# Optimization experiments

Hardware: AMD Instinct MI355X
Metric: run time of the kernel (lower is better)

The kernel has to match this reference:

```python
import jax, jax.numpy as jnp
import numpy as np

GROUP_SIZE = 16777216   # 2**24, output length
PROJ_RATIO = 0.25
INNER = 4194304         # int(GROUP_SIZE * PROJ_RATIO) = 2**22
PADDED = 16777216       # 2**ceil(log2(GROUP_SIZE)) = 2**24
D = 2048                # int(sqrt(INNER))
RANK = 16
ALPHA = 1.0
SCALING = ALPHA / RANK


def setup_inputs() -> dict:
    key = jax.random.key(0)
    kA, kB = jax.random.split(key)
    # LoRA factors (B is zero-init in torch; use small random values so the
    # pipeline produces non-trivial numbers — the math is identical).
    A = jax.random.normal(kA, (RANK, D), dtype=jnp.float32) * 0.02
    Bw = jax.random.normal(kB, (D, RANK), dtype=jnp.float32) * 0.02
    # Fastfood buffers, deterministic as in FastfoodProjection(seed=42)
    rng = np.random.RandomState(42)
    G = jnp.asarray(rng.randn(PADDED), dtype=jnp.float32)
    sign = jnp.asarray(rng.choice([-1, 1], size=PADDED), dtype=jnp.float32)
    perm = jnp.asarray(rng.permutation(PADDED), dtype=jnp.int32)
    return {"A": A, "Bw": Bw, "G": G, "sign": sign, "perm": perm}


def fwht(x):
    """Fast Walsh-Hadamard transform over the last (only) axis, normalized
    by 1/sqrt(n). Same butterfly order as the torch loop: step doubles from 1,
    within each block of 2*step: (a, b) -> (a+b, a-b)."""
    n = x.shape[-1]  # static python int, power of two
    step = 1
    while step < n:
        y = x.reshape(-1, 2, step)               # blocks of 2*step
        x = jnp.concatenate([y[:, :1] + y[:, 1:], y[:, :1] - y[:, 1:]],
                            axis=1).reshape(-1)
        step *= 2
    return x * np.float32(1.0 / np.sqrt(n))


def reference(A, Bw, G, sign, perm):
    # LoRA delta: (D, RANK) @ (RANK, D) * alpha/rank -> (D, D)
    delta = (Bw @ A) * jnp.float32(SCALING)
    flat = delta.reshape(-1)                     # (INNER,)
    flat = jnp.pad(flat, (0, PADDED - INNER))    # zero-pad to 2**24
    # Fastfood: H * G * Pi * H * B
    out = fwht(flat * sign)
    out = out[perm] * G
    out = fwht(out)
    # out_features == GROUP_SIZE == PADDED, so the slice/pad in
    # SuperLoRAGroup.forward is a no-op here; keep it for faithfulness.
    return out[:GROUP_SIZE]
```

## Files before the change

kernel.cpp:

```cpp
#include <hip/hip_runtime.h>


#define THREADS 1024

typedef float vf4 __attribute__((ext_vector_type(4)));
typedef int vi4 __attribute__((ext_vector_type(4)));

constexpr float kScaling = 0.0625f;
constexpr float kNorm = 5.9604644775390625e-8f;

__device__ __forceinline__ void fwht16(float r[16]) {
#pragma unroll
  for (int s = 1; s < 16; s <<= 1) {
#pragma unroll
    for (int i = 0; i < 16; i++) {
      if (!(i & s)) {
        float a = r[i];
        float b = r[i | s];
        r[i] = a + b;
        r[i | s] = a - b;
      }
    }
  }
}

template <bool NT>
__device__ __forceinline__ void fwht_lo_rounds(float* lds, int t, vf4* dst4) {
  vf4* lds4 = (vf4*)lds;
  {
    float r[16];
#pragma unroll
    for (int q = 0; q < 4; q++) {
      vf4 v = lds4[t * 4 + q];
#pragma unroll
      for (int c = 0; c < 4; c++) r[4 * q + c] = v[c];
    }
    fwht16(r);
#pragma unroll
    for (int q = 0; q < 4; q++) {
      vf4 v;
#pragma unroll
      for (int c = 0; c < 4; c++) v[c] = r[4 * q + c];
      lds4[t * 4 + q] = v;
    }
  }
  __syncthreads();
  {
    const int c = (t & 15) | ((t >> 4) << 8);
    float r[16];
#pragma unroll
    for (int k = 0; k < 16; k++) r[k] = lds[c + (k << 4)];
    fwht16(r);
#pragma unroll
    for (int k = 0; k < 16; k++) lds[c + (k << 4)] = r[k];
  }
  __syncthreads();
  {
    const int c = (t & 255) | ((t >> 8) << 12);
    float r[16];
#pragma unroll
    for (int k = 0; k < 16; k++) r[k] = lds[c + (k << 8)];
    fwht16(r);
#pragma unroll
    for (int k = 0; k < 16; k++) lds[c + (k << 8)] = r[k];
  }
  __syncthreads();
  {
    vf4 v0 = lds4[t + 0 * 1024];
    vf4 v1 = lds4[t + 1 * 1024];
    vf4 v2 = lds4[t + 2 * 1024];
    vf4 v3 = lds4[t + 3 * 1024];
    vf4 e0 = v0 + v1, e1 = v0 - v1;
    vf4 e2 = v2 + v3, e3 = v2 - v3;
    vf4 o0 = e0 + e2, o1 = e1 + e3, o2 = e0 - e2, o3 = e1 - e3;
    if (NT) {
      __builtin_nontemporal_store(o0, &dst4[t + 0 * 1024]);
      __builtin_nontemporal_store(o1, &dst4[t + 1 * 1024]);
      __builtin_nontemporal_store(o2, &dst4[t + 2 * 1024]);
      __builtin_nontemporal_store(o3, &dst4[t + 3 * 1024]);
    } else {
      dst4[t + 0 * 1024] = o0;
      dst4[t + 1 * 1024] = o1;
      dst4[t + 2 * 1024] = o2;
      dst4[t + 3 * 1024] = o3;
    }
  }
}

__global__ __launch_bounds__(THREADS) void k1_build_fwht_lo(
    const float* __restrict__ A, const float* __restrict__ Bw,
    const float* __restrict__ sgn, float* __restrict__ W) {
  __shared__ float lds[16384];
  const int t = threadIdx.x;
  const int blk = blockIdx.x;
  const unsigned base = (unsigned)blk << 14;

  float a0[16], a1[16];
#pragma unroll
  for (int k = 0; k < 16; k++) {
    a0[k] = A[k * 2048 + t];
    a1[k] = A[k * 2048 + t + 1024];
  }
  const int r0 = blk * 8;
#pragma unroll
  for (int rl = 0; rl < 8; rl++) {
    float s0 = 0.f, s1 = 0.f;
#pragma unroll
    for (int k = 0; k < 16; k++) {
      float b = Bw[(r0 + rl) * 16 + k];
      s0 += b * a0[k];
      s1 += b * a1[k];
    }
    const int l0 = rl * 2048 + t;
    const int l1 = l0 + 1024;
    lds[l0] = s0 * kScaling * sgn[base + l0];
    lds[l1] = s1 * kScaling * sgn[base + l1];
  }
  __syncthreads();
  fwht_lo_rounds<false>(lds, t, (vf4*)W + ((unsigned)blk << 12));
}

__global__ __launch_bounds__(THREADS) void k_fwht_mid(float* __restrict__ buf) {
  __shared__ float lds[16384];
  vf4* lds4 = (vf4*)lds;
  const int t = threadIdx.x;
  const int seg = blockIdx.x >> 8;
  const int c0 = (blockIdx.x & 255) * 16;
  vf4* B4 = (vf4*)buf + ((unsigned)seg << 20);
#pragma unroll
  for (int m = 0; m < 4; m++) {
    const int idx4 = t + THREADS * m;
    const int row = idx4 >> 4, c4 = idx4 & 15;
    lds4[idx4] = B4[row * 4096 + c0 + c4];
  }
  __syncthreads();
  const int c4 = t & 15;
  const int f = t >> 4;
#pragma unroll
  for (int r = 0; r < 4; r++) {
    const int m = 1 << (2 * r);
    int rows[4];
#pragma unroll
    for (int k2 = 0; k2 < 4; k2++)
      rows[k2] = (f & (m - 1)) + k2 * m + (f >> (2 * r)) * (m << 2);
    vf4 v0 = lds4[rows[0] * 16 + c4];
    vf4 v1 = lds4[rows[1] * 16 + c4];
    vf4 v2 = lds4[rows[2] * 16 + c4];
    vf4 v3 = lds4[rows[3] * 16 + c4];
    vf4 e0 = v0 + v1, e1 = v0 - v1;
    vf4 e2 = v2 + v3, e3 = v2 - v3;
    vf4 o0 = e0 + e2, o1 = e1 + e3, o2 = e0 - e2, o3 = e1 - e3;
    if (r < 3) {
      lds4[rows[0] * 16 + c4] = o0;
      lds4[rows[1] * 16 + c4] = o1;
      lds4[rows[2] * 16 + c4] = o2;
      lds4[rows[3] * 16 + c4] = o3;
      __syncthreads();
    } else {
      B4[rows[0] * 4096 + c0 + c4] = o0;
      B4[rows[1] * 4096 + c0 + c4] = o1;
      B4[rows[2] * 4096 + c0 + c4] = o2;
      B4[rows[3] * 4096 + c0 + c4] = o3;
    }
  }
}

__global__ __launch_bounds__(THREADS) void k3_perm_fwht_lo(
    const float* __restrict__ W, const int* __restrict__ perm,
    const float* __restrict__ G, float* __restrict__ out) {
  __shared__ float lds[16384];
  const int t = threadIdx.x;
  const unsigned base4 = (unsigned)blockIdx.x << 12;
  const vi4* P4 = (const vi4*)perm + base4;
  const vf4* G4 = (const vf4*)G + base4;
  int src[16];
  float gg[16];
#pragma unroll
  for (int m = 0; m < 4; m++) {
    const int idx4 = t + THREADS * m;
    vi4 p = __builtin_nontemporal_load(&P4[idx4]);
    vf4 g = __builtin_nontemporal_load(&G4[idx4]);
#pragma unroll
    for (int c = 0; c < 4; c++) {
      src[4 * m + c] = p[c] & 0x3FFFFF;
      gg[4 * m + c] = g[c] * kNorm;
    }
  }
#pragma unroll
  for (int pass = 0; pass < 4; pass++) {
#pragma unroll
    for (int s = 0; s < 16; s++) {
      if ((src[s] >> 20) == pass) {
        lds[4 * (t + THREADS * (s >> 2)) + (s & 3)] = W[src[s]] * gg[s];
      }
    }
    __syncthreads();
  }
  fwht_lo_rounds<true>(lds, t, (vf4*)out + base4);
}

__global__ __launch_bounds__(THREADS) void k4b_fwht_top(float* __restrict__ out) {
  const unsigned idx4 = blockIdx.x * THREADS + threadIdx.x;
  vf4* O4 = (vf4*)out;
  vf4 v0 = O4[idx4 + 0u * (1u << 20)];
  vf4 v1 = O4[idx4 + 1u * (1u << 20)];
  vf4 v2 = O4[idx4 + 2u * (1u << 20)];
  vf4 v3 = O4[idx4 + 3u * (1u << 20)];
  vf4 e0 = v0 + v1, e1 = v0 - v1;
  vf4 e2 = v2 + v3, e3 = v2 - v3;
  O4[idx4 + 0u * (1u << 20)] = e0 + e2;
  O4[idx4 + 1u * (1u << 20)] = e1 + e3;
  O4[idx4 + 2u * (1u << 20)] = e0 - e2;
  O4[idx4 + 3u * (1u << 20)] = e1 - e3;
}

extern "C" void kernel_launch(void* const* d_in, const int* in_sizes, int n_in,
                              void* d_out, int out_size, void* d_ws,
                              size_t ws_size, hipStream_t stream) {
  (void)in_sizes;
  (void)n_in;
  (void)out_size;
  (void)ws_size;
  const float* A = (const float*)d_in[0];
  const float* Bw = (const float*)d_in[1];
  const float* G = (const float*)d_in[2];
  const float* sgn = (const float*)d_in[3];
  const int* perm = (const int*)d_in[4];
  float* out = (float*)d_out;
  float* W = (float*)d_ws;

  k1_build_fwht_lo<<<256, THREADS, 0, stream>>>(A, Bw, sgn, W);
  k_fwht_mid<<<256, THREADS, 0, stream>>>(W);
  k3_perm_fwht_lo<<<1024, THREADS, 0, stream>>>(W, perm, G, out);
  k_fwht_mid<<<1024, THREADS, 0, stream>>>(out);
  k4b_fwht_top<<<1024, THREADS, 0, stream>>>(out);
}
```

Measured before the change: 361.7 us.

## Fuse upper FWHT stages into one kernel and prefetch W in permute kernel

Merges the mid FWHT pass on the output and the final top radix-4 pass into one kernel, k4_fwht_hi. Each block handles 8 vf4 columns across all four 2^20 segments, keeping results in registers and software-prefetching the next segment's loads. This removes one full read and write of the 64 MB output. In the permute kernel, each block also streams a slice of W per pass into a dummy accumulator, so each W quarter is warmed in cache before the next gather pass, at the cost of extra reads and register pressure.

```diff
diff --git a/kernel.cpp b/kernel.cpp
--- a/kernel.cpp
+++ b/kernel.cpp
@@ -120,13 +120,12 @@
   fwht_lo_rounds<false>(lds, t, (vf4*)W + ((unsigned)blk << 12));
 }
 
-__global__ __launch_bounds__(THREADS) void k_fwht_mid(float* __restrict__ buf) {
+__global__ __launch_bounds__(THREADS) void k2_fwht_mid(float* __restrict__ W) {
   __shared__ float lds[16384];
   vf4* lds4 = (vf4*)lds;
   const int t = threadIdx.x;
-  const int seg = blockIdx.x >> 8;
-  const int c0 = (blockIdx.x & 255) * 16;
-  vf4* B4 = (vf4*)buf + ((unsigned)seg << 20);
+  const int c0 = blockIdx.x * 16;
+  vf4* B4 = (vf4*)W;
 #pragma unroll
   for (int m = 0; m < 4; m++) {
     const int idx4 = t + THREADS * m;
@@ -186,6 +185,17 @@
       gg[4 * m + c] = g[c] * kNorm;
     }
   }
+  const unsigned rank = (blockIdx.x >> 3) & 63;
+  const vf4* Wq = (const vf4*)W;
+  float acc = 0.f;
+  {
+    const unsigned s0 = rank * 4096u + (unsigned)t;
+#pragma unroll
+    for (int i = 0; i < 4; i++) {
+      vf4 v = Wq[s0 + 1024u * i];
+      acc += v[0] + v[1] + v[2] + v[3];
+    }
+  }
 #pragma unroll
   for (int pass = 0; pass < 4; pass++) {
 #pragma unroll
@@ -194,24 +204,89 @@
         lds[4 * (t + THREADS * (s >> 2)) + (s & 3)] = W[src[s]] * gg[s];
       }
     }
+    if (pass < 3) {
+      const unsigned sb =
+          ((unsigned)(pass + 1) << 18) + rank * 4096u + (unsigned)t;
+#pragma unroll
+      for (int i = 0; i < 4; i++) {
+        vf4 v = Wq[sb + 1024u * i];
+        acc += v[0] + v[1] + v[2] + v[3];
+      }
+    }
     __syncthreads();
   }
+  asm volatile("" ::"v"(acc));
   fwht_lo_rounds<true>(lds, t, (vf4*)out + base4);
 }
 
-__global__ __launch_bounds__(THREADS) void k4b_fwht_top(float* __restrict__ out) {
-  const unsigned idx4 = blockIdx.x * THREADS + threadIdx.x;
+__global__ __launch_bounds__(512, 4) void k4_fwht_hi(float* __restrict__ out) {
+  __shared__ float lds[8192];
+  vf4* lds4 = (vf4*)lds;
+  const int t = threadIdx.x;
+  const unsigned c0 = (unsigned)blockIdx.x * 8;
   vf4* O4 = (vf4*)out;
-  vf4 v0 = O4[idx4 + 0u * (1u << 20)];
-  vf4 v1 = O4[idx4 + 1u * (1u << 20)];
-  vf4 v2 = O4[idx4 + 2u * (1u << 20)];
-  vf4 v3 = O4[idx4 + 3u * (1u << 20)];
-  vf4 e0 = v0 + v1, e1 = v0 - v1;
-  vf4 e2 = v2 + v3, e3 = v2 - v3;
-  O4[idx4 + 0u * (1u << 20)] = e0 + e2;
-  O4[idx4 + 1u * (1u << 20)] = e1 + e3;
-  O4[idx4 + 2u * (1u << 20)] = e0 - e2;
-  O4[idx4 + 3u * (1u << 20)] = e1 - e3;
+  const int c4 = t & 7;
+  const int f = t >> 3;
+  vf4 keep[4][4];
+  vf4 ld[4];
+#pragma unroll
+  for (int m = 0; m < 4; m++) {
+    const int idx4 = t + 512 * m;
+    ld[m] = O4[(unsigned)(idx4 >> 3) * 4096u + c0 + (unsigned)(idx4 & 7)];
+  }
+  for (int s = 0; s < 4; s++) {
+#pragma unroll
+    for (int m = 0; m < 4; m++) lds4[t + 512 * m] = ld[m];
+    __syncthreads();
+    if (s < 3) {
+      const unsigned sb = ((unsigned)(s + 1)) << 20;
+#pragma unroll
+      for (int m = 0; m < 4; m++) {
+        const int idx4 = t + 512 * m;
+        ld[m] =
+            O4[sb + (unsigned)(idx4 >> 3) * 4096u + c0 + (unsigned)(idx4 & 7)];
+      }
+    }
+#pragma unroll
+    for (int r = 0; r < 4; r++) {
+      const int m = 1 << (2 * r);
+      int rows[4];
+#pragma unroll
+      for (int k2 = 0; k2 < 4; k2++)
+        rows[k2] = (f & (m - 1)) + k2 * m + (f >> (2 * r)) * (m << 2);
+      vf4 v0 = lds4[rows[0] * 8 + c4];
+      vf4 v1 = lds4[rows[1] * 8 + c4];
+      vf4 v2 = lds4[rows[2] * 8 + c4];
+      vf4 v3 = lds4[rows[3] * 8 + c4];
+      vf4 e0 = v0 + v1, e1 = v0 - v1;
+      vf4 e2 = v2 + v3, e3 = v2 - v3;
+      vf4 o0 = e0 + e2, o1 = e1 + e3, o2 = e0 - e2, o3 = e1 - e3;
+      if (r < 3) {
+        lds4[rows[0] * 8 + c4] = o0;
+        lds4[rows[1] * 8 + c4] = o1;
+        lds4[rows[2] * 8 + c4] = o2;
+        lds4[rows[3] * 8 + c4] = o3;
+        __syncthreads();
+      } else {
+        keep[s][0] = o0;
+        keep[s][1] = o1;
+        keep[s][2] = o2;
+        keep[s][3] = o3;
+      }
+    }
+    __syncthreads();
+  }
+#pragma unroll
+  for (int k2 = 0; k2 < 4; k2++) {
+    vf4 v0 = keep[0][k2], v1 = keep[1][k2], v2 = keep[2][k2], v3 = keep[3][k2];
+    vf4 e0 = v0 + v1, e1 = v0 - v1;
+    vf4 e2 = v2 + v3, e3 = v2 - v3;
+    const unsigned base = (unsigned)(f + 64 * k2) * 4096u + c0 + (unsigned)c4;
+    __builtin_nontemporal_store(e0 + e2, &O4[base + (0u << 20)]);
+    __builtin_nontemporal_store(e1 + e3, &O4[base + (1u << 20)]);
+    __builtin_nontemporal_store(e0 - e2, &O4[base + (2u << 20)]);
+    __builtin_nontemporal_store(e1 - e3, &O4[base + (3u << 20)]);
+  }
 }
 
 extern "C" void kernel_launch(void* const* d_in, const int* in_sizes, int n_in,
@@ -230,8 +305,7 @@
   float* W = (float*)d_ws;
 
   k1_build_fwht_lo<<<256, THREADS, 0, stream>>>(A, Bw, sgn, W);
-  k_fwht_mid<<<256, THREADS, 0, stream>>>(W);
+  k2_fwht_mid<<<256, THREADS, 0, stream>>>(W);
   k3_perm_fwht_lo<<<1024, THREADS, 0, stream>>>(W, perm, G, out);
-  k_fwht_mid<<<1024, THREADS, 0, stream>>>(out);
-  k4b_fwht_top<<<1024, THREADS, 0, stream>>>(out);
-}
+  k4_fwht_hi<<<512, 512, 0, stream>>>(out);
+}
```

Result: slower. 378.7 us (+4.7%).

## Replace LDS-based mid/top FWHT kernels with register-only strided streaming passes

Applied to the files above, without the earlier changes.

Removes the shared-memory mid-FWHT kernel and the separate top-round kernel. In their place is a templated kernel in which each thread loads 16 or 32 strided float4s into registers, runs a radix-16/32 butterfly, and writes back, with no LDS and no barriers. The workspace now takes two such passes instead of one LDS pass. The output still takes two passes, the last one using nontemporal stores. This trades LDS traffic and synchronisation for more global round-trips on the workspace, smaller grids, and higher register use per thread.

```diff
diff --git a/kernel.cpp b/kernel.cpp
--- a/kernel.cpp
+++ b/kernel.cpp
@@ -120,48 +120,34 @@
   fwht_lo_rounds<false>(lds, t, (vf4*)W + ((unsigned)blk << 12));
 }
 
-__global__ __launch_bounds__(THREADS) void k_fwht_mid(float* __restrict__ buf) {
-  __shared__ float lds[16384];
-  vf4* lds4 = (vf4*)lds;
-  const int t = threadIdx.x;
-  const int seg = blockIdx.x >> 8;
-  const int c0 = (blockIdx.x & 255) * 16;
-  vf4* B4 = (vf4*)buf + ((unsigned)seg << 20);
-#pragma unroll
-  for (int m = 0; m < 4; m++) {
-    const int idx4 = t + THREADS * m;
-    const int row = idx4 >> 4, c4 = idx4 & 15;
-    lds4[idx4] = B4[row * 4096 + c0 + c4];
-  }
-  __syncthreads();
-  const int c4 = t & 15;
-  const int f = t >> 4;
-#pragma unroll
-  for (int r = 0; r < 4; r++) {
-    const int m = 1 << (2 * r);
-    int rows[4];
-#pragma unroll
-    for (int k2 = 0; k2 < 4; k2++)
-      rows[k2] = (f & (m - 1)) + k2 * m + (f >> (2 * r)) * (m << 2);
-    vf4 v0 = lds4[rows[0] * 16 + c4];
-    vf4 v1 = lds4[rows[1] * 16 + c4];
-    vf4 v2 = lds4[rows[2] * 16 + c4];
-    vf4 v3 = lds4[rows[3] * 16 + c4];
-    vf4 e0 = v0 + v1, e1 = v0 - v1;
-    vf4 e2 = v2 + v3, e3 = v2 - v3;
-    vf4 o0 = e0 + e2, o1 = e1 + e3, o2 = e0 - e2, o3 = e1 - e3;
-    if (r < 3) {
-      lds4[rows[0] * 16 + c4] = o0;
-      lds4[rows[1] * 16 + c4] = o1;
-      lds4[rows[2] * 16 + c4] = o2;
-      lds4[rows[3] * 16 + c4] = o3;
-      __syncthreads();
-    } else {
-      B4[rows[0] * 4096 + c0 + c4] = o0;
-      B4[rows[1] * 4096 + c0 + c4] = o1;
-      B4[rows[2] * 4096 + c0 + c4] = o2;
-      B4[rows[3] * 4096 + c0 + c4] = o3;
-    }
+template <int RLOG, int LOWLOG, bool NTST>
+__global__ __launch_bounds__(256) void k_stream_fwht(float* __restrict__ buf) {
+  constexpr int R = 1 << RLOG;
+  vf4* B4 = (vf4*)buf;
+  const unsigned idx = blockIdx.x * 256u + threadIdx.x;
+  const unsigned low = idx & ((1u << LOWLOG) - 1u);
+  const unsigned high = idx >> LOWLOG;
+  const unsigned base = (high << (LOWLOG + RLOG)) | low;
+  vf4 r[R];
+#pragma unroll
+  for (int m = 0; m < R; m++) r[m] = B4[base + ((unsigned)m << LOWLOG)];
+#pragma unroll
+  for (int s = 1; s < R; s <<= 1) {
+#pragma unroll
+    for (int i = 0; i < R; i++) {
+      if (!(i & s)) {
+        vf4 a = r[i], b = r[i | s];
+        r[i] = a + b;
+        r[i | s] = a - b;
+      }
+    }
+  }
+#pragma unroll
+  for (int m = 0; m < R; m++) {
+    if (NTST)
+      __builtin_nontemporal_store(r[m], &B4[base + ((unsigned)m << LOWLOG)]);
+    else
+      B4[base + ((unsigned)m << LOWLOG)] = r[m];
   }
 }
 
@@ -197,21 +183,6 @@
     __syncthreads();
   }
   fwht_lo_rounds<true>(lds, t, (vf4*)out + base4);
-}
-
-__global__ __launch_bounds__(THREADS) void k4b_fwht_top(float* __restrict__ out) {
-  const unsigned idx4 = blockIdx.x * THREADS + threadIdx.x;
-  vf4* O4 = (vf4*)out;
-  vf4 v0 = O4[idx4 + 0u * (1u << 20)];
-  vf4 v1 = O4[idx4 + 1u * (1u << 20)];
-  vf4 v2 = O4[idx4 + 2u * (1u << 20)];
-  vf4 v3 = O4[idx4 + 3u * (1u << 20)];
-  vf4 e0 = v0 + v1, e1 = v0 - v1;
-  vf4 e2 = v2 + v3, e3 = v2 - v3;
-  O4[idx4 + 0u * (1u << 20)] = e0 + e2;
-  O4[idx4 + 1u * (1u << 20)] = e1 + e3;
-  O4[idx4 + 2u * (1u << 20)] = e0 - e2;
-  O4[idx4 + 3u * (1u << 20)] = e1 - e3;
 }
 
 extern "C" void kernel_launch(void* const* d_in, const int* in_sizes, int n_in,
@@ -230,8 +201,9 @@
   float* W = (float*)d_ws;
 
   k1_build_fwht_lo<<<256, THREADS, 0, stream>>>(A, Bw, sgn, W);
-  k_fwht_mid<<<256, THREADS, 0, stream>>>(W);
+  k_stream_fwht<4, 12, false><<<256, 256, 0, stream>>>(W);
+  k_stream_fwht<4, 16, false><<<256, 256, 0, stream>>>(W);
   k3_perm_fwht_lo<<<1024, THREADS, 0, stream>>>(W, perm, G, out);
-  k_fwht_mid<<<1024, THREADS, 0, stream>>>(out);
-  k4b_fwht_top<<<1024, THREADS, 0, stream>>>(out);
-}
+  k_stream_fwht<5, 12, false><<<512, 256, 0, stream>>>(out);
+  k_stream_fwht<5, 17, true><<<512, 256, 0, stream>>>(out);
+}
```

Result: no change. 366.2 us (+1.3%).
